# Performance work log

Measured on AMD Instinct MI355X. Metric: run time of the kernel, lower is better.

Reference implementation:

```python
import jax, jax.numpy as jnp
import numpy as np

CH = 256            # channels
IN_C = CH // 2      # 128
INTER_C = CH // 16  # 16
NUM_POINTS = 32
BN_EPS = 1e-5


def conv1x1(x, W, b=None):
    # x: [B,C,H,W], W: [O,C]
    y = jnp.einsum('oc,bchw->bohw', W, x)
    if b is not None:
        y = y + b[None, :, None, None]
    return y


def bilinear_sample(feat, sx, sy):
    """feat [B,C,H,W]; sx,sy [B,N,P] continuous index coords; border padding."""
    B, C, H, W = feat.shape
    x0f = jnp.floor(sx)
    y0f = jnp.floor(sy)
    wx = sx - x0f
    wy = sy - y0f
    x0 = jnp.clip(x0f.astype(jnp.int32), 0, W - 1)
    x1 = jnp.clip(x0f.astype(jnp.int32) + 1, 0, W - 1)
    y0 = jnp.clip(y0f.astype(jnp.int32), 0, H - 1)
    y1 = jnp.clip(y0f.astype(jnp.int32) + 1, 0, H - 1)
    feat_f = feat.reshape(B, C, H * W).transpose(0, 2, 1)  # [B,HW,C]

    def gather(yi, xi):
        idx = (yi * W + xi).reshape(B, -1)  # [B,N*P]
        return jnp.take_along_axis(feat_f, idx[:, :, None], axis=1)  # [B,N*P,C]

    wxf = wx.reshape(B, -1, 1)
    wyf = wy.reshape(B, -1, 1)
    out = (gather(y0, x0) * (1 - wxf) * (1 - wyf)
           + gather(y0, x1) * wxf * (1 - wyf)
           + gather(y1, x0) * (1 - wxf) * wyf
           + gather(y1, x1) * wxf * wyf)
    N, P = sx.shape[1], sx.shape[2]
    return out.reshape(B, N, P, C)


def multi_scale_attention(qf, vf, Wq, bq, Wk, bk, Wv, bv, Woff, boff):
    # deformable-style point-sampling attention with NUM_POINTS samples per query
    B, _, H, W = qf.shape
    N = H * W
    q = conv1x1(qf, Wq, bq).reshape(B, INTER_C, N).transpose(0, 2, 1)  # [B,N,Ci]
    k = conv1x1(vf, Wk, bk)                                            # [B,Ci,H,W]
    v = conv1x1(vf, Wv, bv)                                            # [B,Cv,H,W]
    off = conv1x1(qf, Woff, boff).reshape(B, NUM_POINTS, 2, N)
    off = off.transpose(0, 3, 1, 2)                                    # [B,N,P,2] (dx,dy)
    ys, xs = jnp.meshgrid(jnp.arange(H, dtype=qf.dtype),
                          jnp.arange(W, dtype=qf.dtype), indexing='ij')
    sx = xs.reshape(-1)[None, :, None] + off[..., 0]                   # [B,N,P]
    sy = ys.reshape(-1)[None, :, None] + off[..., 1]
    k_s = bilinear_sample(k, sx, sy)                                   # [B,N,P,Ci]
    v_s = bilinear_sample(v, sx, sy)                                   # [B,N,P,Cv]
    logits = jnp.einsum('bnc,bnpc->bnp', q, k_s) / jnp.sqrt(jnp.asarray(INTER_C, qf.dtype))
    attn = jax.nn.softmax(logits, axis=-1)
    out = jnp.einsum('bnp,bnpc->bnc', attn, v_s)                       # [B,N,Cv]
    return out.transpose(0, 2, 1).reshape(B, -1, H, W)


def setup_inputs() -> dict:
    key = jax.random.key(0)
    ks = jax.random.split(key, 12)
    B, Hl, Wl, Hh, Wh = 2, 64, 64, 32, 32
    s = 0.02
    return {
        'low_feature': jax.random.normal(ks[0], (B, CH, Hl, Wl), jnp.float32),
        'high_feature': jax.random.normal(ks[1], (B, CH, Hh, Wh), jnp.float32),
        'W1': jax.random.normal(ks[2], (IN_C, 2 * CH), jnp.float32) * s,
        'b1': jnp.zeros((IN_C,), jnp.float32),
        'W2': jax.random.normal(ks[3], (IN_C, CH), jnp.float32) * s,
        'b2': jnp.zeros((IN_C,), jnp.float32),
        'Wq': jax.random.normal(ks[4], (INTER_C, IN_C), jnp.float32) * s,
        'bq': jnp.zeros((INTER_C,), jnp.float32),
        'Wk': jax.random.normal(ks[5], (INTER_C, IN_C), jnp.float32) * s,
        'bk': jnp.zeros((INTER_C,), jnp.float32),
        'Wv': jax.random.normal(ks[6], (IN_C, IN_C), jnp.float32) * s,
        'bv': jnp.zeros((IN_C,), jnp.float32),
        'Woff': jax.random.normal(ks[7], (2 * NUM_POINTS, IN_C), jnp.float32) * 0.5,
        'boff': jnp.zeros((2 * NUM_POINTS,), jnp.float32),
        'Wb': jax.random.normal(ks[8], (CH, IN_C + CH), jnp.float32) * s,
        'gamma': jnp.ones((CH,), jnp.float32),
        'beta': jnp.zeros((CH,), jnp.float32),
        'rmean': jnp.zeros((CH,), jnp.float32),
        'rvar': jnp.ones((CH,), jnp.float32),
    }


def reference(low_feature, high_feature, W1, b1, W2, b2, Wq, bq, Wk, bk,
              Wv, bv, Woff, boff, Wb, gamma, beta, rmean, rvar):
    B, _, Hl, Wl = low_feature.shape
    # F.interpolate(mode='bilinear', align_corners=False) == jax.image half-pixel bilinear
    high_up = jax.image.resize(high_feature, (B, CH, Hl, Wl), method='bilinear')
    query_feature = conv1x1(jnp.concatenate([high_up, low_feature], axis=1), W1, b1)
    value_feature = conv1x1(high_up, W2, b2)
    value_feature = multi_scale_attention(query_feature, value_feature,
                                          Wq, bq, Wk, bk, Wv, bv, Woff, boff)
    x = conv1x1(jnp.concatenate([value_feature, high_up], axis=1), Wb)
    # BatchNorm (eval form) + ReLU
    x = (x - rmean[None, :, None, None]) * jax.lax.rsqrt(rvar + BN_EPS)[None, :, None, None]
    x = x * gamma[None, :, None, None] + beta[None, :, None, None]
    return jax.nn.relu(x)
```

## Files before the change

kernel.cpp:

```cpp
#include <hip/hip_runtime.h>
#include <hip/hip_bf16.h>

#define NL 4096
#define HH 32
#define WH 32

typedef __attribute__((ext_vector_type(8))) short s8v;
typedef __attribute__((ext_vector_type(4))) short s4v;
typedef __attribute__((ext_vector_type(4))) float f32x4;

static __device__ inline unsigned short f2bf(float x) {
  __hip_bfloat16 h = __float2bfloat16(x);
  return *reinterpret_cast<unsigned short*>(&h);
}
static __device__ inline float bfbits2f(unsigned int lo16) {
  unsigned int u = lo16 << 16;
  return *reinterpret_cast<float*>(&u);
}

static __device__ inline int swizzle_wg(int b) {
  return ((b & 7) << 6) | (b >> 3);
}

__global__ __launch_bounds__(256) void convert_weights_k(
    const float* __restrict__ w1, const float* __restrict__ w2,
    const float* __restrict__ wq, const float* __restrict__ woff,
    const float* __restrict__ wk, const float* __restrict__ wv,
    const float* __restrict__ wb, short* __restrict__ dst) {
  int i = (blockIdx.x * 256 + threadIdx.x) * 4;
  const float* src; int off;
  if      (i <  65536) { src = w1;   off = 0; }
  else if (i <  98304) { src = w2;   off = 65536; }
  else if (i < 100352) { src = wq;   off = 98304; }
  else if (i < 108544) { src = woff; off = 100352; }
  else if (i < 110592) { src = wk;   off = 108544; }
  else if (i < 126976) { src = wv;   off = 110592; }
  else if (i < 225280) { src = wb;   off = 126976; }
  else return;
  float4 v = *(const float4*)(src + (i - off));
  s4v o;
  o[0] = (short)f2bf(v.x); o[1] = (short)f2bf(v.y);
  o[2] = (short)f2bf(v.z); o[3] = (short)f2bf(v.w);
  *(s4v*)(dst + i) = o;
}

__global__ __launch_bounds__(512, 4) void k1_fused(
    const float* __restrict__ low, const float* __restrict__ high,
    const short* __restrict__ wc,
    const float* __restrict__ b1, const float* __restrict__ b2,
    const float* __restrict__ bq, const float* __restrict__ boff,
    const float* __restrict__ bk, const float* __restrict__ bv,
    short* __restrict__ xh, float* __restrict__ q_t, float* __restrict__ k_t,
    float* __restrict__ off_t, short* __restrict__ v_t) {
  __shared__ short xin_s[16 * 520];
  __shared__ short qf_s[16 * 136];
  __shared__ short vf_s[16 * 136];
  const int tid = threadIdx.x;
  const int wg = swizzle_wg(blockIdx.x);
  const int pix0 = wg * 16;
  const int b = pix0 >> 12;
  const int n0 = pix0 & (NL - 1);

  {
    const int nl = tid & 15, cg = tid >> 4;
    const int n = n0 + nl;
    const int y = n >> 6, x = n & 63;
    float sx = x * 0.5f - 0.25f;
    float sy = y * 0.5f - 0.25f;
    float x0f = floorf(sx), y0f = floorf(sy);
    float wx = sx - x0f, wy = sy - y0f;
    int x0i = (int)x0f, y0i = (int)y0f;
    int x0c = min(WH - 1, max(0, x0i)), x1c = min(WH - 1, max(0, x0i + 1));
    int y0c = min(HH - 1, max(0, y0i)), y1c = min(HH - 1, max(0, y0i + 1));
    float w00 = (1.f - wy) * (1.f - wx), w01 = (1.f - wy) * wx;
    float w10 = wy * (1.f - wx),         w11 = wy * wx;
#pragma unroll
    for (int i = 0; i < 8; i++) {
      int c = cg * 8 + i;
      const float* f = high + (size_t)(b * 256 + c) * (HH * WH);
      float v = w00 * f[y0c * WH + x0c] + w01 * f[y0c * WH + x1c]
              + w10 * f[y1c * WH + x0c] + w11 * f[y1c * WH + x1c];
      xin_s[nl * 520 + c] = (short)f2bf(v);
      xin_s[nl * 520 + 256 + c] =
          (short)f2bf(low[(size_t)(b * 256 + c) * NL + n]);
    }
  }
  __syncthreads();

  {
    const int r = tid >> 5, c0 = (tid & 31) * 8;
    s8v v0 = *(const s8v*)(xin_s + r * 520 + c0);
    *(s8v*)(xh + (size_t)(pix0 + r) * 256 + c0) = v0;
  }

  const int wave = tid >> 6, lane = tid & 63;
  const int quad = lane >> 4, id = lane & 15;

  {
    f32x4 acc = (f32x4){0.f, 0.f, 0.f, 0.f};
    const short* a0 = wc + (size_t)(wave * 16 + id) * 512 + quad * 8;
    const short* bp = xin_s + id * 520 + quad * 8;
#pragma unroll
    for (int kk = 0; kk < 512; kk += 32)
      acc = __builtin_amdgcn_mfma_f32_16x16x32_bf16(
          *(const s8v*)(a0 + kk), *(const s8v*)(bp + kk), acc, 0, 0, 0);
    int m0 = wave * 16 + quad * 4;
    s4v o0;
#pragma unroll
    for (int r = 0; r < 4; r++) o0[r] = (short)f2bf(acc[r] + b1[m0 + r]);
    *(s4v*)(qf_s + id * 136 + m0) = o0;
  }

  {
    f32x4 acc = (f32x4){0.f, 0.f, 0.f, 0.f};
    const short* a0 = wc + 65536 + (size_t)(wave * 16 + id) * 256 + quad * 8;
    const short* bp = xin_s + id * 520 + quad * 8;
#pragma unroll
    for (int kk = 0; kk < 256; kk += 32)
      acc = __builtin_amdgcn_mfma_f32_16x16x32_bf16(
          *(const s8v*)(a0 + kk), *(const s8v*)(bp + kk), acc, 0, 0, 0);
    int m0 = wave * 16 + quad * 4;
    s4v o0;
#pragma unroll
    for (int r = 0; r < 4; r++) o0[r] = (short)f2bf(acc[r] + b2[m0 + r]);
    *(s4v*)(vf_s + id * 136 + m0) = o0;
  }
  __syncthreads();

  for (int f = wave; f < 14; f += 8) {
    const short* ap = wc + 98304 + (size_t)(f * 16 + id) * 128 + quad * 8;
    const short* bp = (f < 5 ? qf_s : vf_s) + id * 136 + quad * 8;
    f32x4 acc = (f32x4){0.f, 0.f, 0.f, 0.f};
#pragma unroll
    for (int kk = 0; kk < 128; kk += 32)
      acc = __builtin_amdgcn_mfma_f32_16x16x32_bf16(
          *(const s8v*)(ap + kk), *(const s8v*)(bp + kk), acc, 0, 0, 0);
    const int pix = pix0 + id;
    const int mq = quad * 4;
    if (f == 0) {
      f32x4 v;
#pragma unroll
      for (int r = 0; r < 4; r++) v[r] = acc[r] + bq[mq + r];
      *(f32x4*)(q_t + (size_t)pix * 16 + mq) = v;
    } else if (f < 5) {
      int m = (f - 1) * 16 + mq;
      f32x4 v;
#pragma unroll
      for (int r = 0; r < 4; r++) v[r] = acc[r] + boff[m + r];
      *(f32x4*)(off_t + (size_t)pix * 64 + m) = v;
    } else if (f == 5) {
      f32x4 v;
#pragma unroll
      for (int r = 0; r < 4; r++) v[r] = acc[r] + bk[mq + r];
      *(f32x4*)(k_t + (size_t)pix * 16 + mq) = v;
    } else {
      int m = (f - 6) * 16 + mq;
      s4v o;
#pragma unroll
      for (int r = 0; r < 4; r++) o[r] = (short)f2bf(acc[r] + bv[m + r]);
      *(s4v*)(v_t + (size_t)pix * 128 + m) = o;
    }
  }
}

__global__ __launch_bounds__(1024, 2) void k2_fused(
    const float* __restrict__ q_t, const float* __restrict__ k_t,
    const short* __restrict__ v_t, const float* __restrict__ off_t,
    const short* __restrict__ xh, const short* __restrict__ wb,
    const float* __restrict__ gamma, const float* __restrict__ beta,
    const float* __restrict__ rmean, const float* __restrict__ rvar,
    float* __restrict__ out) {
  __shared__ float2 s_wi[16][32][4];
  __shared__ short attn_s[16 * 136];
  const int tid = threadIdx.x;
  const int wave = tid >> 6, lane = tid & 63;
  const int wg = swizzle_wg(blockIdx.x);
  const int pix0 = wg * 16;

  {
    const int qidx = pix0 + wave;
    const int b = qidx >> 12;
    const int n = qidx & (NL - 1);
    const int qy = n >> 6, qx = n & 63;

    const float* qp = q_t + (size_t)qidx * 16;
    float qreg[16];
#pragma unroll
    for (int i = 0; i < 16; i += 4) {
      float4 t = *(const float4*)(qp + i);
      qreg[i] = t.x; qreg[i + 1] = t.y; qreg[i + 2] = t.z; qreg[i + 3] = t.w;
    }

    const int pt = lane >> 1, h = lane & 1;
    float2 dxy = *(const float2*)(off_t + (size_t)qidx * 64 + 2 * pt);
    float sx = (float)qx + dxy.x;
    float sy = (float)qy + dxy.y;
    float x0f = floorf(sx), y0f = floorf(sy);
    float wx = sx - x0f, wy = sy - y0f;
    int x0i = (int)x0f, y0i = (int)y0f;
    int x0 = min(63, max(0, x0i)), x1 = min(63, max(0, x0i + 1));
    int y0 = min(63, max(0, y0i)), y1 = min(63, max(0, y0i + 1));

    int   yr  = h ? y1 : y0;
    float wyr = h ? wy : (1.f - wy);
    int   pa = yr * 64 + x0, pb = yr * 64 + x1;
    float wa = wyr * (1.f - wx), wb_ = wyr * wx;

    const float* kb = k_t + (size_t)b * NL * 16;
    float da = 0.f, db = 0.f;
    {
      const float* ka = kb + (size_t)pa * 16;
      const float* kc = kb + (size_t)pb * 16;
#pragma unroll
      for (int i = 0; i < 16; i += 4) {
        float4 a4 = *(const float4*)(ka + i);
        float4 c4 = *(const float4*)(kc + i);
        da = fmaf(qreg[i], a4.x, da); da = fmaf(qreg[i + 1], a4.y, da);
        da = fmaf(qreg[i + 2], a4.z, da); da = fmaf(qreg[i + 3], a4.w, da);
        db = fmaf(qreg[i], c4.x, db); db = fmaf(qreg[i + 1], c4.y, db);
        db = fmaf(qreg[i + 2], c4.z, db); db = fmaf(qreg[i + 3], c4.w, db);
      }
    }
    float part = wa * da + wb_ * db;
    part += __shfl_xor(part, 1, 64);
    float logit = part * 0.25f;

    float m = logit;
#pragma unroll
    for (int s = 32; s > 0; s >>= 1) m = fmaxf(m, __shfl_xor(m, s, 64));
    float e = __expf(logit - m);
    float ssum = e;
#pragma unroll
    for (int s = 32; s > 0; s >>= 1) ssum += __shfl_xor(ssum, s, 64);
    float a = e * 2.f / ssum;

    s_wi[wave][pt][2 * h + 0] = make_float2(a * wa,  __int_as_float(pa));
    s_wi[wave][pt][2 * h + 1] = make_float2(a * wb_, __int_as_float(pb));

    const int t = lane >> 4, chunk = lane & 15;
    const short* vb = v_t + (size_t)b * NL * 128 + chunk * 8;
    float o[8];
#pragma unroll
    for (int j = 0; j < 8; j++) o[j] = 0.f;
#pragma unroll
    for (int pp = 0; pp < 32; pp++) {
      float2 wi = s_wi[wave][pp][t];
      float w_ = wi.x;
      int  pix = __float_as_int(wi.y);
      uint4 u = *(const uint4*)(vb + (size_t)pix * 128);
      o[0] = fmaf(w_, bfbits2f(u.x & 0xffffu), o[0]);
      o[1] = fmaf(w_, bfbits2f(u.x >> 16),     o[1]);
      o[2] = fmaf(w_, bfbits2f(u.y & 0xffffu), o[2]);
      o[3] = fmaf(w_, bfbits2f(u.y >> 16),     o[3]);
      o[4] = fmaf(w_, bfbits2f(u.z & 0xffffu), o[4]);
      o[5] = fmaf(w_, bfbits2f(u.z >> 16),     o[5]);
      o[6] = fmaf(w_, bfbits2f(u.w & 0xffffu), o[6]);
      o[7] = fmaf(w_, bfbits2f(u.w >> 16),     o[7]);
    }
#pragma unroll
    for (int j = 0; j < 8; j++) {
      o[j] += __shfl_xor(o[j], 16, 64);
      o[j] += __shfl_xor(o[j], 32, 64);
    }
    if (t == 0) {
      uint4 pk;
      pk.x = (unsigned)f2bf(o[0]) | ((unsigned)f2bf(o[1]) << 16);
      pk.y = (unsigned)f2bf(o[2]) | ((unsigned)f2bf(o[3]) << 16);
      pk.z = (unsigned)f2bf(o[4]) | ((unsigned)f2bf(o[5]) << 16);
      pk.w = (unsigned)f2bf(o[6]) | ((unsigned)f2bf(o[7]) << 16);
      *(uint4*)(attn_s + wave * 136 + chunk * 8) = pk;
    }
  }
  __syncthreads();

  {
    const int quad = lane >> 4, id = lane & 15;
    const int m0 = wave * 16;
    const int pix = pix0 + id;

    f32x4 acc = (f32x4){0.f, 0.f, 0.f, 0.f};
    const short* ap = wb + (size_t)(m0 + id) * 384 + quad * 8;
    const short* bs = attn_s + id * 136 + quad * 8;
    const short* bg = xh + (size_t)pix * 256 + quad * 8;
#pragma unroll
    for (int k = 0; k < 4; k++)
      acc = __builtin_amdgcn_mfma_f32_16x16x32_bf16(
          *(const s8v*)(ap + k * 32), *(const s8v*)(bs + k * 32), acc, 0, 0, 0);
#pragma unroll
    for (int k = 0; k < 8; k++)
      acc = __builtin_amdgcn_mfma_f32_16x16x32_bf16(
          *(const s8v*)(ap + 128 + k * 32), *(const s8v*)(bg + k * 32), acc, 0, 0, 0);

    const int bb = pix >> 12, nlow = pix & (NL - 1);
    const int mbase = m0 + quad * 4;
#pragma unroll
    for (int r = 0; r < 4; r++) {
      int o = mbase + r;
      float s  = gamma[o] * rsqrtf(rvar[o] + 1e-5f);
      float sh = beta[o] - rmean[o] * s;
      __builtin_nontemporal_store(fmaxf(fmaf(acc[r], s, sh), 0.f),
                                  &out[((size_t)bb * 256 + o) * NL + nlow]);
    }
  }
}

extern "C" void kernel_launch(void* const* d_in, const int* in_sizes, int n_in,
                              void* d_out, int out_size, void* d_ws, size_t ws_size,
                              hipStream_t stream) {
  const float* low   = (const float*)d_in[0];
  const float* high  = (const float*)d_in[1];
  const float* W1    = (const float*)d_in[2];
  const float* b1    = (const float*)d_in[3];
  const float* W2    = (const float*)d_in[4];
  const float* b2    = (const float*)d_in[5];
  const float* Wq    = (const float*)d_in[6];
  const float* bq    = (const float*)d_in[7];
  const float* Wk    = (const float*)d_in[8];
  const float* bk    = (const float*)d_in[9];
  const float* Wv    = (const float*)d_in[10];
  const float* bv    = (const float*)d_in[11];
  const float* Woff  = (const float*)d_in[12];
  const float* boff  = (const float*)d_in[13];
  const float* Wb    = (const float*)d_in[14];
  const float* gamma = (const float*)d_in[15];
  const float* beta  = (const float*)d_in[16];
  const float* rmean = (const float*)d_in[17];
  const float* rvar  = (const float*)d_in[18];
  float* out = (float*)d_out;

  short* ws    = (short*)d_ws;
  short* xh    = ws;
  short* v_t   = xh + 2097152;
  short* wc    = v_t + 1048576;
  float* q_t   = (float*)(wc + 225280);
  float* k_t   = q_t + 131072;
  float* off_t = k_t + 131072;

  convert_weights_k<<<220, 256, 0, stream>>>(W1, W2, Wq, Woff, Wk, Wv, Wb, wc);
  k1_fused<<<512, 512, 0, stream>>>(low, high, wc, b1, b2, bq, boff, bk, bv,
                                    xh, q_t, k_t, off_t, v_t);
  k2_fused<<<512, 1024, 0, stream>>>(q_t, k_t, v_t, off_t, xh, wc + 126976,
                                     gamma, beta, rmean, rvar, out);
}
```

Before: 152.5 us.

## Fuse three kernels into one cooperative kernel with grid-wide syncs

Result: slower. 256.0 us (+67.9%).

```diff
diff --git a/kernel.cpp b/kernel.cpp
--- a/kernel.cpp
+++ b/kernel.cpp
@@ -1,5 +1,8 @@
 #include <hip/hip_runtime.h>
 #include <hip/hip_bf16.h>
+#include <hip/hip_cooperative_groups.h>
+
+namespace cg = cooperative_groups;
 
 #define NL 4096
 #define HH 32
@@ -17,9 +20,303 @@
   unsigned int u = lo16 << 16;
   return *reinterpret_cast<float*>(&u);
 }
-
 static __device__ inline int swizzle_wg(int b) {
   return ((b & 7) << 6) | (b >> 3);
+}
+
+__global__ __launch_bounds__(512, 4) void fused_all(
+    const float* __restrict__ low, const float* __restrict__ high,
+    const float* __restrict__ w1f, const float* __restrict__ w2f,
+    const float* __restrict__ wqf, const float* __restrict__ wofff,
+    const float* __restrict__ wkf, const float* __restrict__ wvf,
+    const float* __restrict__ wbf,
+    const float* __restrict__ b1, const float* __restrict__ b2,
+    const float* __restrict__ bq, const float* __restrict__ boff,
+    const float* __restrict__ bk, const float* __restrict__ bv,
+    const float* __restrict__ gamma, const float* __restrict__ beta,
+    const float* __restrict__ rmean, const float* __restrict__ rvar,
+    short* __restrict__ wc, short* __restrict__ xh,
+    float* __restrict__ q_t, float* __restrict__ k_t,
+    float* __restrict__ off_t, short* __restrict__ v_t,
+    float* __restrict__ out) {
+  __shared__ __align__(16) char smraw[25344];
+  short* xin_s = (short*)smraw;
+  short* qf_s  = (short*)(smraw + 16640);
+  short* vf_s  = (short*)(smraw + 20992);
+  float2* s_wi = (float2*)smraw;
+  short* attn_s = (short*)(smraw + 16384);
+
+  const int tid  = threadIdx.x;
+  const int bidx = blockIdx.x;
+  cg::grid_group grid = cg::this_grid();
+
+  {
+    int i = (bidx * 512 + tid) * 4;
+    if (i < 225280) {
+      const float* src; int off;
+      if      (i <  65536) { src = w1f;   off = 0; }
+      else if (i <  98304) { src = w2f;   off = 65536; }
+      else if (i < 100352) { src = wqf;   off = 98304; }
+      else if (i < 108544) { src = wofff; off = 100352; }
+      else if (i < 110592) { src = wkf;   off = 108544; }
+      else if (i < 126976) { src = wvf;   off = 110592; }
+      else                 { src = wbf;   off = 126976; }
+      float4 v = *(const float4*)(src + (i - off));
+      s4v o;
+      o[0] = (short)f2bf(v.x); o[1] = (short)f2bf(v.y);
+      o[2] = (short)f2bf(v.z); o[3] = (short)f2bf(v.w);
+      *(s4v*)(wc + i) = o;
+    }
+  }
+  grid.sync();
+
+  const int xcd = bidx & 7, slot = bidx >> 3;
+  const int wave = tid >> 6, lane = tid & 63;
+  const int quad = lane >> 4, id = lane & 15;
+
+  for (int tt = 0; tt < 2; tt++) {
+    const int wg = xcd * 64 + slot * 2 + tt;
+    const int pix0 = wg * 16;
+    const int b = pix0 >> 12;
+    const int n0 = pix0 & (NL - 1);
+
+    {
+      const int nl = tid & 15, cgp = tid >> 4;
+      const int n = n0 + nl;
+      const int y = n >> 6, x = n & 63;
+      float sx = x * 0.5f - 0.25f;
+      float sy = y * 0.5f - 0.25f;
+      float x0f = floorf(sx), y0f = floorf(sy);
+      float wx = sx - x0f, wy = sy - y0f;
+      int x0i = (int)x0f, y0i = (int)y0f;
+      int x0c = min(WH - 1, max(0, x0i)), x1c = min(WH - 1, max(0, x0i + 1));
+      int y0c = min(HH - 1, max(0, y0i)), y1c = min(HH - 1, max(0, y0i + 1));
+      float w00 = (1.f - wy) * (1.f - wx), w01 = (1.f - wy) * wx;
+      float w10 = wy * (1.f - wx),         w11 = wy * wx;
+#pragma unroll
+      for (int i = 0; i < 8; i++) {
+        int c = cgp * 8 + i;
+        const float* f = high + (size_t)(b * 256 + c) * (HH * WH);
+        float v = w00 * f[y0c * WH + x0c] + w01 * f[y0c * WH + x1c]
+                + w10 * f[y1c * WH + x0c] + w11 * f[y1c * WH + x1c];
+        xin_s[nl * 520 + c] = (short)f2bf(v);
+        xin_s[nl * 520 + 256 + c] =
+            (short)f2bf(low[(size_t)(b * 256 + c) * NL + n]);
+      }
+    }
+    __syncthreads();
+
+    {
+      const int r = tid >> 5, c0 = (tid & 31) * 8;
+      s8v v0 = *(const s8v*)(xin_s + r * 520 + c0);
+      *(s8v*)(xh + (size_t)(pix0 + r) * 256 + c0) = v0;
+    }
+
+    {
+      f32x4 acc = (f32x4){0.f, 0.f, 0.f, 0.f};
+      const short* a0 = wc + (size_t)(wave * 16 + id) * 512 + quad * 8;
+      const short* bp = xin_s + id * 520 + quad * 8;
+#pragma unroll
+      for (int kk = 0; kk < 512; kk += 32)
+        acc = __builtin_amdgcn_mfma_f32_16x16x32_bf16(
+            *(const s8v*)(a0 + kk), *(const s8v*)(bp + kk), acc, 0, 0, 0);
+      int m0 = wave * 16 + quad * 4;
+      s4v o0;
+#pragma unroll
+      for (int r = 0; r < 4; r++) o0[r] = (short)f2bf(acc[r] + b1[m0 + r]);
+      *(s4v*)(qf_s + id * 136 + m0) = o0;
+    }
+
+    {
+      f32x4 acc = (f32x4){0.f, 0.f, 0.f, 0.f};
+      const short* a0 = wc + 65536 + (size_t)(wave * 16 + id) * 256 + quad * 8;
+      const short* bp = xin_s + id * 520 + quad * 8;
+#pragma unroll
+      for (int kk = 0; kk < 256; kk += 32)
+        acc = __builtin_amdgcn_mfma_f32_16x16x32_bf16(
+            *(const s8v*)(a0 + kk), *(const s8v*)(bp + kk), acc, 0, 0, 0);
+      int m0 = wave * 16 + quad * 4;
+      s4v o0;
+#pragma unroll
+      for (int r = 0; r < 4; r++) o0[r] = (short)f2bf(acc[r] + b2[m0 + r]);
+      *(s4v*)(vf_s + id * 136 + m0) = o0;
+    }
+    __syncthreads();
+
+    for (int f = wave; f < 14; f += 8) {
+      const short* ap = wc + 98304 + (size_t)(f * 16 + id) * 128 + quad * 8;
+      const short* bp = (f < 5 ? qf_s : vf_s) + id * 136 + quad * 8;
+      f32x4 acc = (f32x4){0.f, 0.f, 0.f, 0.f};
+#pragma unroll
+      for (int kk = 0; kk < 128; kk += 32)
+        acc = __builtin_amdgcn_mfma_f32_16x16x32_bf16(
+            *(const s8v*)(ap + kk), *(const s8v*)(bp + kk), acc, 0, 0, 0);
+      const int pix = pix0 + id;
+      const int mq = quad * 4;
+      if (f == 0) {
+        f32x4 v;
+#pragma unroll
+        for (int r = 0; r < 4; r++) v[r] = acc[r] + bq[mq + r];
+        *(f32x4*)(q_t + (size_t)pix * 16 + mq) = v;
+      } else if (f < 5) {
+        int m = (f - 1) * 16 + mq;
+        f32x4 v;
+#pragma unroll
+        for (int r = 0; r < 4; r++) v[r] = acc[r] + boff[m + r];
+        *(f32x4*)(off_t + (size_t)pix * 64 + m) = v;
+      } else if (f == 5) {
+        f32x4 v;
+#pragma unroll
+        for (int r = 0; r < 4; r++) v[r] = acc[r] + bk[mq + r];
+        *(f32x4*)(k_t + (size_t)pix * 16 + mq) = v;
+      } else {
+        int m = (f - 6) * 16 + mq;
+        s4v o;
+#pragma unroll
+        for (int r = 0; r < 4; r++) o[r] = (short)f2bf(acc[r] + bv[m + r]);
+        *(s4v*)(v_t + (size_t)pix * 128 + m) = o;
+      }
+    }
+    __syncthreads();
+  }
+
+  grid.sync();
+
+  const short* wcb = wc + 126976;
+  for (int tt = 0; tt < 2; tt++) {
+    const int pix0 = (xcd * 64 + slot * 2 + tt) * 16;
+
+#pragma unroll
+    for (int qi = 0; qi < 2; qi++) {
+      const int ql = wave + 8 * qi;
+      const int qidx = pix0 + ql;
+      const int bt = qidx >> 12;
+      const int n = qidx & (NL - 1);
+      const int qy = n >> 6, qx = n & 63;
+
+      const float* qp = q_t + (size_t)qidx * 16;
+      float qreg[16];
+#pragma unroll
+      for (int i = 0; i < 16; i += 4) {
+        float4 t4 = *(const float4*)(qp + i);
+        qreg[i] = t4.x; qreg[i + 1] = t4.y; qreg[i + 2] = t4.z; qreg[i + 3] = t4.w;
+      }
+
+      const int pt = lane >> 1, h = lane & 1;
+      float2 dxy = *(const float2*)(off_t + (size_t)qidx * 64 + 2 * pt);
+      float sx = (float)qx + dxy.x;
+      float sy = (float)qy + dxy.y;
+      float x0f = floorf(sx), y0f = floorf(sy);
+      float wx = sx - x0f, wy = sy - y0f;
+      int x0i = (int)x0f, y0i = (int)y0f;
+      int x0 = min(63, max(0, x0i)), x1 = min(63, max(0, x0i + 1));
+      int y0 = min(63, max(0, y0i)), y1 = min(63, max(0, y0i + 1));
+
+      int   yr  = h ? y1 : y0;
+      float wyr = h ? wy : (1.f - wy);
+      int   pa = yr * 64 + x0, pb = yr * 64 + x1;
+      float wa = wyr * (1.f - wx), wb_ = wyr * wx;
+
+      const float* kb = k_t + (size_t)bt * NL * 16;
+      float da = 0.f, db = 0.f;
+      {
+        const float* ka = kb + (size_t)pa * 16;
+        const float* kc = kb + (size_t)pb * 16;
+#pragma unroll
+        for (int i = 0; i < 16; i += 4) {
+          float4 a4 = *(const float4*)(ka + i);
+          float4 c4 = *(const float4*)(kc + i);
+          da = fmaf(qreg[i], a4.x, da); da = fmaf(qreg[i + 1], a4.y, da);
+          da = fmaf(qreg[i + 2], a4.z, da); da = fmaf(qreg[i + 3], a4.w, da);
+          db = fmaf(qreg[i], c4.x, db); db = fmaf(qreg[i + 1], c4.y, db);
+          db = fmaf(qreg[i + 2], c4.z, db); db = fmaf(qreg[i + 3], c4.w, db);
+        }
+      }
+      float part = wa * da + wb_ * db;
+      part += __shfl_xor(part, 1, 64);
+      float logit = part * 0.25f;
+
+      float m = logit;
+#pragma unroll
+      for (int s = 32; s > 0; s >>= 1) m = fmaxf(m, __shfl_xor(m, s, 64));
+      float e = __expf(logit - m);
+      float ssum = e;
+#pragma unroll
+      for (int s = 32; s > 0; s >>= 1) ssum += __shfl_xor(ssum, s, 64);
+      float a = e * 2.f / ssum;
+
+      s_wi[(ql * 32 + pt) * 4 + 2 * h + 0] =
+          make_float2(a * wa,  __int_as_float(pa << 7));
+      s_wi[(ql * 32 + pt) * 4 + 2 * h + 1] =
+          make_float2(a * wb_, __int_as_float(pb << 7));
+
+      const int t = lane >> 4, chunk = lane & 15;
+      const short* vb = v_t + (size_t)bt * NL * 128 + chunk * 8;
+      float o[8];
+#pragma unroll
+      for (int j = 0; j < 8; j++) o[j] = 0.f;
+#pragma unroll
+      for (int pp = 0; pp < 32; pp++) {
+        float2 wi = s_wi[(ql * 32 + pp) * 4 + t];
+        float w_ = wi.x;
+        int  offs = __float_as_int(wi.y);
+        uint4 u = *(const uint4*)(vb + offs);
+        o[0] = fmaf(w_, bfbits2f(u.x & 0xffffu), o[0]);
+        o[1] = fmaf(w_, bfbits2f(u.x >> 16),     o[1]);
+        o[2] = fmaf(w_, bfbits2f(u.y & 0xffffu), o[2]);
+        o[3] = fmaf(w_, bfbits2f(u.y >> 16),     o[3]);
+        o[4] = fmaf(w_, bfbits2f(u.z & 0xffffu), o[4]);
+        o[5] = fmaf(w_, bfbits2f(u.z >> 16),     o[5]);
+        o[6] = fmaf(w_, bfbits2f(u.w & 0xffffu), o[6]);
+        o[7] = fmaf(w_, bfbits2f(u.w >> 16),     o[7]);
+      }
+#pragma unroll
+      for (int j = 0; j < 8; j++) {
+        o[j] += __shfl_xor(o[j], 16, 64);
+        o[j] += __shfl_xor(o[j], 32, 64);
+      }
+      if (t == 0) {
+        uint4 pk;
+        pk.x = (unsigned)f2bf(o[0]) | ((unsigned)f2bf(o[1]) << 16);
+        pk.y = (unsigned)f2bf(o[2]) | ((unsigned)f2bf(o[3]) << 16);
+        pk.z = (unsigned)f2bf(o[4]) | ((unsigned)f2bf(o[5]) << 16);
+        pk.w = (unsigned)f2bf(o[6]) | ((unsigned)f2bf(o[7]) << 16);
+        *(uint4*)(attn_s + ql * 136 + chunk * 8) = pk;
+      }
+    }
+    __syncthreads();
+
+#pragma unroll
+    for (int j = 0; j < 2; j++) {
+      const int m0 = wave * 16 + j * 128;
+      const int pix = pix0 + id;
+
+      f32x4 acc = (f32x4){0.f, 0.f, 0.f, 0.f};
+      const short* ap = wcb + (size_t)(m0 + id) * 384 + quad * 8;
+      const short* bs = attn_s + id * 136 + quad * 8;
+      const short* bg = xh + (size_t)pix * 256 + quad * 8;
+#pragma unroll
+      for (int k = 0; k < 4; k++)
+        acc = __builtin_amdgcn_mfma_f32_16x16x32_bf16(
+            *(const s8v*)(ap + k * 32), *(const s8v*)(bs + k * 32), acc, 0, 0, 0);
+#pragma unroll
+      for (int k = 0; k < 8; k++)
+        acc = __builtin_amdgcn_mfma_f32_16x16x32_bf16(
+            *(const s8v*)(ap + 128 + k * 32), *(const s8v*)(bg + k * 32), acc, 0, 0, 0);
+
+      const int bb = pix >> 12, nlow = pix & (NL - 1);
+      const int mbase = m0 + quad * 4;
+#pragma unroll
+      for (int r = 0; r < 4; r++) {
+        int oo = mbase + r;
+        float s  = gamma[oo] * rsqrtf(rvar[oo] + 1e-5f);
+        float sh = beta[oo] - rmean[oo] * s;
+        __builtin_nontemporal_store(fmaxf(fmaf(acc[r], s, sh), 0.f),
+                                    &out[((size_t)bb * 256 + oo) * NL + nlow]);
+      }
+    }
+    __syncthreads();
+  }
 }
 
 __global__ __launch_bounds__(256) void convert_weights_k(
@@ -60,7 +357,6 @@
   const int pix0 = wg * 16;
   const int b = pix0 >> 12;
   const int n0 = pix0 & (NL - 1);
-
   {
     const int nl = tid & 15, cg = tid >> 4;
     const int n = n0 + nl;
@@ -86,16 +382,13 @@
     }
   }
   __syncthreads();
-
   {
     const int r = tid >> 5, c0 = (tid & 31) * 8;
     s8v v0 = *(const s8v*)(xin_s + r * 520 + c0);
     *(s8v*)(xh + (size_t)(pix0 + r) * 256 + c0) = v0;
   }
-
   const int wave = tid >> 6, lane = tid & 63;
   const int quad = lane >> 4, id = lane & 15;
-
   {
     f32x4 acc = (f32x4){0.f, 0.f, 0.f, 0.f};
     const short* a0 = wc + (size_t)(wave * 16 + id) * 512 + quad * 8;
@@ -110,7 +403,6 @@
     for (int r = 0; r < 4; r++) o0[r] = (short)f2bf(acc[r] + b1[m0 + r]);
     *(s4v*)(qf_s + id * 136 + m0) = o0;
   }
-
   {
     f32x4 acc = (f32x4){0.f, 0.f, 0.f, 0.f};
     const short* a0 = wc + 65536 + (size_t)(wave * 16 + id) * 256 + quad * 8;
@@ -126,7 +418,6 @@
     *(s4v*)(vf_s + id * 136 + m0) = o0;
   }
   __syncthreads();
-
   for (int f = wave; f < 14; f += 8) {
     const short* ap = wc + 98304 + (size_t)(f * 16 + id) * 128 + quad * 8;
     const short* bp = (f < 5 ? qf_s : vf_s) + id * 136 + quad * 8;
@@ -176,13 +467,11 @@
   const int wave = tid >> 6, lane = tid & 63;
   const int wg = swizzle_wg(blockIdx.x);
   const int pix0 = wg * 16;
-
   {
     const int qidx = pix0 + wave;
     const int b = qidx >> 12;
     const int n = qidx & (NL - 1);
     const int qy = n >> 6, qx = n & 63;
-
     const float* qp = q_t + (size_t)qidx * 16;
     float qreg[16];
 #pragma unroll
@@ -190,7 +479,6 @@
       float4 t = *(const float4*)(qp + i);
       qreg[i] = t.x; qreg[i + 1] = t.y; qreg[i + 2] = t.z; qreg[i + 3] = t.w;
     }
-
     const int pt = lane >> 1, h = lane & 1;
     float2 dxy = *(const float2*)(off_t + (size_t)qidx * 64 + 2 * pt);
     float sx = (float)qx + dxy.x;
@@ -200,12 +488,10 @@
     int x0i = (int)x0f, y0i = (int)y0f;
     int x0 = min(63, max(0, x0i)), x1 = min(63, max(0, x0i + 1));
     int y0 = min(63, max(0, y0i)), y1 = min(63, max(0, y0i + 1));
-
     int   yr  = h ? y1 : y0;
     float wyr = h ? wy : (1.f - wy);
     int   pa = yr * 64 + x0, pb = yr * 64 + x1;
     float wa = wyr * (1.f - wx), wb_ = wyr * wx;
-
     const float* kb = k_t + (size_t)b * NL * 16;
     float da = 0.f, db = 0.f;
     {
@@ -224,7 +510,6 @@
     float part = wa * da + wb_ * db;
     part += __shfl_xor(part, 1, 64);
     float logit = part * 0.25f;
-
     float m = logit;
 #pragma unroll
     for (int s = 32; s > 0; s >>= 1) m = fmaxf(m, __shfl_xor(m, s, 64));
@@ -233,10 +518,8 @@
 #pragma unroll
     for (int s = 32; s > 0; s >>= 1) ssum += __shfl_xor(ssum, s, 64);
     float a = e * 2.f / ssum;
-
     s_wi[wave][pt][2 * h + 0] = make_float2(a * wa,  __int_as_float(pa));
     s_wi[wave][pt][2 * h + 1] = make_float2(a * wb_, __int_as_float(pb));
-
     const int t = lane >> 4, chunk = lane & 15;
     const short* vb = v_t + (size_t)b * NL * 128 + chunk * 8;
     float o[8];
@@ -272,12 +555,10 @@
     }
   }
   __syncthreads();
-
   {
     const int quad = lane >> 4, id = lane & 15;
     const int m0 = wave * 16;
     const int pix = pix0 + id;
-
     f32x4 acc = (f32x4){0.f, 0.f, 0.f, 0.f};
     const short* ap = wb + (size_t)(m0 + id) * 384 + quad * 8;
     const short* bs = attn_s + id * 136 + quad * 8;
@@ -290,7 +571,6 @@
     for (int k = 0; k < 8; k++)
       acc = __builtin_amdgcn_mfma_f32_16x16x32_bf16(
           *(const s8v*)(ap + 128 + k * 32), *(const s8v*)(bg + k * 32), acc, 0, 0, 0);
-
     const int bb = pix >> 12, nlow = pix & (NL - 1);
     const int mbase = m0 + quad * 4;
 #pragma unroll
@@ -336,9 +616,22 @@
   float* k_t   = q_t + 131072;
   float* off_t = k_t + 131072;
 
-  convert_weights_k<<<220, 256, 0, stream>>>(W1, W2, Wq, Woff, Wk, Wv, Wb, wc);
-  k1_fused<<<512, 512, 0, stream>>>(low, high, wc, b1, b2, bq, boff, bk, bv,
-                                    xh, q_t, k_t, off_t, v_t);
-  k2_fused<<<512, 1024, 0, stream>>>(q_t, k_t, v_t, off_t, xh, wc + 126976,
-                                     gamma, beta, rmean, rvar, out);
-}
+  void* args[] = {
+      (void*)&low, (void*)&high, (void*)&W1, (void*)&W2, (void*)&Wq,
+      (void*)&Woff, (void*)&Wk, (void*)&Wv, (void*)&Wb,
+      (void*)&b1, (void*)&b2, (void*)&bq, (void*)&boff, (void*)&bk, (void*)&bv,
+      (void*)&gamma, (void*)&beta, (void*)&rmean, (void*)&rvar,
+      (void*)&wc, (void*)&xh, (void*)&q_t, (void*)&k_t, (void*)&off_t,
+      (void*)&v_t, (void*)&out};
+  hipError_t err = hipLaunchCooperativeKernel(
+      reinterpret_cast<const void*>(&fused_all), dim3(256), dim3(512),
+      args, 0, stream);
+  if (err != hipSuccess) {
+    (void)hipGetLastError();
+    convert_weights_k<<<220, 256, 0, stream>>>(W1, W2, Wq, Woff, Wk, Wv, Wb, wc);
+    k1_fused<<<512, 512, 0, stream>>>(low, high, wc, b1, b2, bq, boff, bk, bv,
+                                      xh, q_t, k_t, off_t, v_t);
+    k2_fused<<<512, 1024, 0, stream>>>(q_t, k_t, v_t, off_t, xh, wc + 126976,
+                                       gamma, beta, rmean, rvar, out);
+  }
+}
```
